# Performance work log

Hardware: AMD Instinct MI355X
Metric: run time of the kernel (lower is better)

Reference implementation:

```python
import jax, jax.numpy as jnp
import numpy as np
from jax import lax

B, C_IN, H = 64, 3, 64
K_FEAT, KSIZE, STRIDE = 24, 8, 8
G_IN, G_HID, F_HID, OUT = 52, 256, 256, 1


def setup_inputs() -> dict:
    key = jax.random.key(0)
    ks = jax.random.split(key, 8)
    s = lambda fan_in: 1.0 / np.sqrt(fan_in)
    return {
        "image": jax.random.normal(ks[0], (B, C_IN, H, H), jnp.float32),
        "conv_w": jax.random.normal(ks[1], (K_FEAT, C_IN, KSIZE, KSIZE), jnp.float32) * s(C_IN * KSIZE * KSIZE),
        "conv_b": jnp.zeros((K_FEAT,), jnp.float32),
        "g_w1": jax.random.normal(ks[2], (G_IN, G_HID), jnp.float32) * s(G_IN),
        "g_b1": jnp.zeros((G_HID,), jnp.float32),
        "g_w2": jax.random.normal(ks[3], (G_HID, G_HID), jnp.float32) * s(G_HID),
        "g_b2": jnp.zeros((G_HID,), jnp.float32),
        "f_w1": jax.random.normal(ks[4], (G_HID, F_HID), jnp.float32) * s(G_HID),
        "f_b1": jnp.zeros((F_HID,), jnp.float32),
        "f_w2": jax.random.normal(ks[5], (F_HID, OUT), jnp.float32) * s(F_HID),
        "f_b2": jnp.zeros((OUT,), jnp.float32),
    }


def reference(image, conv_w, conv_b, g_w1, g_b1, g_w2, g_b2, f_w1, f_b1, f_w2, f_b2):
    # feature_extractor: conv k8/s8 + ReLU -> (B, k, d, d)
    x = lax.conv_general_dilated(image, conv_w, (STRIDE, STRIDE), "VALID",
                                 dimension_numbers=("NCHW", "OIHW", "NCHW"))
    x = jax.nn.relu(x + conv_b[None, :, None, None])
    b, k, d, _ = x.shape
    # coordinate channels: x varies along columns, y along rows (linspace(-1,1,d))
    coord = jnp.linspace(-1.0, 1.0, d, dtype=x.dtype)
    cx = jnp.broadcast_to(coord[None, None, None, :], (b, 1, d, d))
    cy = jnp.broadcast_to(coord[None, None, :, None], (b, 1, d, d))
    x = jnp.concatenate([x, cx, cy], axis=1)          # (B, k+2, d, d)
    k2 = k + 2
    x = x.reshape(b, k2, d * d).transpose(0, 2, 1)     # (B, d^2, k+2)
    # all-pairs: pair (i, j) -> concat(x[:, j], x[:, i])  (matches repeat/cat in torch)
    left = jnp.broadcast_to(x[:, None, :, :], (b, d * d, d * d, k2))
    right = jnp.broadcast_to(x[:, :, None, :], (b, d * d, d * d, k2))
    pairs = jnp.concatenate([left, right], axis=-1)    # (B, d^2, d^2, 2(k+2))
    # g: shared MLP over pairs
    h = jax.nn.relu(pairs @ g_w1 + g_b1)
    h = jax.nn.relu(h @ g_w2 + g_b2)                   # (B, d^2, d^2, 256)
    pooled = jnp.sum(h, axis=(1, 2))                   # sum over d^4 pairs -> (B, 256)
    # f: head MLP
    h = jax.nn.relu(pooled @ f_w1 + f_b1)
    return h @ f_w2 + f_b2                             # (B, 1)
```

## Files before the change

### kernel.cpp

```cpp
#include <hip/hip_runtime.h>
#include <hip/hip_bf16.h>
#include <stdint.h>


typedef float f32x4 __attribute__((ext_vector_type(4)));
typedef float f32x2 __attribute__((ext_vector_type(2)));
typedef short short8 __attribute__((ext_vector_type(8)));
typedef int   int4v  __attribute__((ext_vector_type(4)));

__device__ __forceinline__ uint32_t cvt_pk_bf16(float lo, float hi) {
    uint32_t r;
    asm("v_cvt_pk_bf16_f32 %0, %1, %2" : "=v"(r) : "v"(lo), "v"(hi));
    return r;
}
__device__ __forceinline__ f32x2 relu2(f32x2 a) {
    f32x2 z = (f32x2){0.f, 0.f};
    return __builtin_elementwise_max(a, z);
}

__global__ void k12_front(const float* __restrict__ img, const float* __restrict__ cw,
                          const float* __restrict__ cb, const float* __restrict__ w1,
                          const float* __restrict__ b1, const float* __restrict__ w2,
                          float* __restrict__ u, float* __restrict__ v,
                          short* __restrict__ w2f) {
    int g = blockIdx.x;
    int t = threadIdx.x;
    if (g >= 256) {
        int fi = (g - 256) * 4 + (t >> 6);
        int l = t & 63;
        int ks = fi >> 4, ni2 = fi & 15;
        int n  = ni2 * 16 + (l & 15);
        int k0 = ks * 32 + (l >> 4) * 8;
        float f[8];
        #pragma unroll
        for (int e = 0; e < 8; ++e) f[e] = w2[(k0 + e) * 256 + n];
        union { short8 s; uint32_t w[4]; } A;
        A.w[0] = cvt_pk_bf16(f[0], f[1]);
        A.w[1] = cvt_pk_bf16(f[2], f[3]);
        A.w[2] = cvt_pk_bf16(f[4], f[5]);
        A.w[3] = cvt_pk_bf16(f[6], f[7]);
        *(short8*)(w2f + (fi * 64 + l) * 8) = A.s;
        return;
    }
    __shared__ float xs[16][26];
    int b = g >> 2, q = g & 3, p0 = q * 16;

    for (int idx = t; idx < 416; idx += 256) {
        int pl = idx / 26;
        int ch = idx - pl * 26;
        int pos = p0 + pl;
        int r = pos >> 3, c = pos & 7;
        float val;
        if (ch < 24) {
            float s = cb[ch];
            #pragma unroll
            for (int ci = 0; ci < 3; ++ci)
                #pragma unroll
                for (int kr = 0; kr < 8; ++kr) {
                    const float* ip = img + ((b * 3 + ci) * 64 + r * 8 + kr) * 64 + c * 8;
                    const float* wp = cw + ((ch * 3 + ci) * 8 + kr) * 8;
                    #pragma unroll
                    for (int kc = 0; kc < 8; ++kc) s += ip[kc] * wp[kc];
                }
            val = fmaxf(s, 0.f);
        } else if (ch == 24) {
            val = -1.f + (2.f / 7.f) * (float)c;
        } else {
            val = -1.f + (2.f / 7.f) * (float)r;
        }
        xs[pl][ch] = val;
    }
    __syncthreads();

    int c = t;
    float bc = b1[c];
    float su[16], sv[16];
    #pragma unroll
    for (int r = 0; r < 16; ++r) { su[r] = bc; sv[r] = 0.f; }
    #pragma unroll 2
    for (int k = 0; k < 26; ++k) {
        float wu = w1[k * 256 + c];
        float wv2 = w1[(26 + k) * 256 + c];
        #pragma unroll
        for (int r = 0; r < 16; ++r) {
            float xv = xs[r][k];
            su[r] += xv * wu;
            sv[r] += xv * wv2;
        }
    }
    #pragma unroll
    for (int r = 0; r < 16; ++r) {
        int bj = b * 64 + p0 + r;
        u[bj * 256 + c] = su[r];
        v[bj * 256 + c] = sv[r];
    }
}

#define STAGE_ALL(VSROW, WB)                                           \
{                                                                      \
    f32x4 va = *(const f32x4*)&vs[VSROW][col16 * 8];                   \
    f32x4 vb = *(const f32x4*)&vs[VSROW][col16 * 8 + 4];               \
    _Pragma("unroll 4")                                                \
    for (int p = 0; p < 8; ++p) {                                      \
        f32x4 x0 = *(const f32x4*)(uth + p * 2048);                    \
        f32x4 x1 = *(const f32x4*)(uth + p * 2048 + 4);                \
        f32x2 a0 = relu2((f32x2){x0.x, x0.y} + (f32x2){va.x, va.y});   \
        f32x2 a1 = relu2((f32x2){x0.z, x0.w} + (f32x2){va.z, va.w});   \
        f32x2 a2 = relu2((f32x2){x1.x, x1.y} + (f32x2){vb.x, vb.y});   \
        f32x2 a3 = relu2((f32x2){x1.z, x1.w} + (f32x2){vb.z, vb.w});   \
        int4v d;                                                       \
        d.x = (int)cvt_pk_bf16(a0.x, a0.y);                            \
        d.y = (int)cvt_pk_bf16(a1.x, a1.y);                            \
        d.z = (int)cvt_pk_bf16(a2.x, a2.y);                            \
        d.w = (int)cvt_pk_bf16(a3.x, a3.y);                            \
        *(int4v*)((WB) + p * 4096) = d;                                \
    }                                                                  \
}

#define MFMA_ROW(AV, MI, KS)                                                                    \
      acc[MI][0] = __builtin_amdgcn_mfma_f32_16x16x32_bf16(AV, Bf[KS][0], acc[MI][0], 0, 0, 0); \
      acc[MI][1] = __builtin_amdgcn_mfma_f32_16x16x32_bf16(AV, Bf[KS][1], acc[MI][1], 0, 0, 0); \
      acc[MI][2] = __builtin_amdgcn_mfma_f32_16x16x32_bf16(AV, Bf[KS][2], acc[MI][2], 0, 0, 0); \
      acc[MI][3] = __builtin_amdgcn_mfma_f32_16x16x32_bf16(AV, Bf[KS][3], acc[MI][3], 0, 0, 0);

#define MFMA_KS(KS)                                                   \
    { const char* hx = ((KS) & 1) ? hO : hE;                          \
      short8 a0 = *(const short8*)(hx + ((KS) >> 1) * 128);           \
      short8 a1 = *(const short8*)(hx + 8192  + ((KS) >> 1) * 128);   \
      short8 a2 = *(const short8*)(hx + 16384 + ((KS) >> 1) * 128);   \
      short8 a3 = *(const short8*)(hx + 24576 + ((KS) >> 1) * 128);   \
      MFMA_ROW(a0, 0, KS) MFMA_ROW(a1, 1, KS)                         \
      MFMA_ROW(a2, 2, KS) MFMA_ROW(a3, 3, KS) }

__global__ __launch_bounds__(256, 2) void k3_pairs(
        const float* __restrict__ u, const float* __restrict__ v,
        const short* __restrict__ w2f, const float* __restrict__ b2,
        float* __restrict__ part) {
    __shared__ short h1s[2][64 * 256];
    __shared__ float vs[8][256];
    int t = threadIdx.x;
    int lane = t & 63, wv = t >> 6;
    int lr = lane & 15, lg = lane >> 4;
    int blk = blockIdx.x;
    int b = blk & 63, i0 = (blk >> 6) * 8;
    bool late = (blk >> 8) & 1;

    {
        int q = t >> 5, c8 = (t & 31) * 8;
        const float* vr = v + (b * 64 + i0 + q) * 256 + c8;
        *(float4*)&vs[q][c8]     = *(const float4*)vr;
        *(float4*)&vs[q][c8 + 4] = *(const float4*)(vr + 4);
    }

    short8 Bf[8][4];
    #pragma unroll
    for (int ks = 0; ks < 8; ++ks)
        #pragma unroll
        for (int cg = 0; cg < 4; ++cg)
            Bf[ks][cg] = *(const short8*)(w2f + ((ks * 16 + wv * 4 + cg) * 64 + lane) * 8);

    f32x2 bias2[4];
    #pragma unroll
    for (int cg = 0; cg < 4; ++cg) {
        float bv = b2[wv * 64 + cg * 16 + lr];
        bias2[cg] = (f32x2){bv, bv};
    }

    int col16 = t & 31, rowbase = t >> 5;
    const float* uth = u + (b * 64 + rowbase) * 256 + col16 * 8;
    int wbase = rowbase * 512 + ((col16 * 16) ^ (rowbase << 4));
    int xb = (lg * 16) ^ ((lr & 7) << 4);
    int rE = lr * 512 + xb;
    int rO = lr * 512 + (xb ^ 64);

    __syncthreads();
    STAGE_ALL(0, (char*)h1s[0] + wbase)
    __syncthreads();

    f32x2 csum2[4];
    #pragma unroll
    for (int cg = 0; cg < 4; ++cg) csum2[cg] = (f32x2){0.f, 0.f};

    #pragma unroll 1
    for (int qq = 0; qq < 8; ++qq) {
        const char* hE = (const char*)h1s[qq & 1] + rE;
        const char* hO = (const char*)h1s[qq & 1] + rO;
        char* wb = (char*)h1s[(qq & 1) ^ 1] + wbase;

        f32x4 acc[4][4];
        #pragma unroll
        for (int mi = 0; mi < 4; ++mi)
            #pragma unroll
            for (int cg = 0; cg < 4; ++cg) acc[mi][cg] = (f32x4){0.f, 0.f, 0.f, 0.f};

        if (!late) {
            if (qq < 7) STAGE_ALL(qq + 1, wb)
            __builtin_amdgcn_s_setprio(1);
            MFMA_KS(0) MFMA_KS(1) MFMA_KS(2) MFMA_KS(3)
            MFMA_KS(4) MFMA_KS(5) MFMA_KS(6) MFMA_KS(7)
            __builtin_amdgcn_s_setprio(0);
        } else {
            __builtin_amdgcn_s_setprio(1);
            MFMA_KS(0) MFMA_KS(1) MFMA_KS(2) MFMA_KS(3)
            __builtin_amdgcn_s_setprio(0);
            if (qq < 7) STAGE_ALL(qq + 1, wb)
            __builtin_amdgcn_s_setprio(1);
            MFMA_KS(4) MFMA_KS(5) MFMA_KS(6) MFMA_KS(7)
            __builtin_amdgcn_s_setprio(0);
        }

        #pragma unroll
        for (int cg = 0; cg < 4; ++cg) {
            #pragma unroll
            for (int mi = 0; mi < 4; ++mi) {
                f32x2 lo = relu2((f32x2){acc[mi][cg].x, acc[mi][cg].y} + bias2[cg]);
                f32x2 hi = relu2((f32x2){acc[mi][cg].z, acc[mi][cg].w} + bias2[cg]);
                csum2[cg] = csum2[cg] + lo + hi;
            }
        }
        __syncthreads();
    }

    #pragma unroll
    for (int cg = 0; cg < 4; ++cg) {
        float s = csum2[cg].x + csum2[cg].y;
        s += __shfl_xor(s, 16);
        s += __shfl_xor(s, 32);
        if (lane < 16) part[blk * 256 + wv * 64 + cg * 16 + lr] = s;
    }
}

__global__ void k5_head(const float* __restrict__ part, const float* __restrict__ fw1,
                        const float* __restrict__ fb1, const float* __restrict__ fw2,
                        const float* __restrict__ fb2, float* __restrict__ out) {
    __shared__ float P[256];
    __shared__ float wsum[4];
    int b = blockIdx.x, t = threadIdx.x;
    float s0 = 0.f;
    #pragma unroll
    for (int g = 0; g < 8; ++g) s0 += part[(b + 64 * g) * 256 + t];
    P[t] = s0;
    __syncthreads();
    float a0 = 0.f, a1 = 0.f, a2 = 0.f, a3 = 0.f;
    for (int k = 0; k < 64; ++k) {
        a0 += P[k]       * fw1[k * 256 + t];
        a1 += P[k + 64]  * fw1[(k + 64) * 256 + t];
        a2 += P[k + 128] * fw1[(k + 128) * 256 + t];
        a3 += P[k + 192] * fw1[(k + 192) * 256 + t];
    }
    float h = fmaxf(fb1[t] + a0 + a1 + a2 + a3, 0.f);
    float p = h * fw2[t];
    #pragma unroll
    for (int off = 32; off >= 1; off >>= 1) p += __shfl_xor(p, off);
    if ((t & 63) == 0) wsum[t >> 6] = p;
    __syncthreads();
    if (t == 0) out[b] = wsum[0] + wsum[1] + wsum[2] + wsum[3] + fb2[0];
}

extern "C" void kernel_launch(void* const* d_in, const int* in_sizes, int n_in,
                              void* d_out, int out_size, void* d_ws, size_t ws_size,
                              hipStream_t stream) {
    const float* image  = (const float*)d_in[0];
    const float* conv_w = (const float*)d_in[1];
    const float* conv_b = (const float*)d_in[2];
    const float* g_w1   = (const float*)d_in[3];
    const float* g_b1   = (const float*)d_in[4];
    const float* g_w2   = (const float*)d_in[5];
    const float* g_b2   = (const float*)d_in[6];
    const float* f_w1   = (const float*)d_in[7];
    const float* f_b1   = (const float*)d_in[8];
    const float* f_w2   = (const float*)d_in[9];
    const float* f_b2   = (const float*)d_in[10];
    float* out = (float*)d_out;

    char* ws = (char*)d_ws;
    float* u    = (float*)(ws + 0);
    float* v    = (float*)(ws + 4194304);
    short* w2f  = (short*)(ws + 8388608);
    float* part = (float*)(ws + 8519680);

    k12_front<<<288, 256, 0, stream>>>(image, conv_w, conv_b, g_w1, g_b1, g_w2,
                                       u, v, w2f);
    k3_pairs<<<512, 256, 0, stream>>>(u, v, w2f, g_b2, part);
    k5_head<<<64, 256, 0, stream>>>(part, f_w1, f_b1, f_w2, f_b2, out);
}
```

Before: 66.39 us.

## Restructure pair kernel into 512-thread blocks with register-cached u rows

```diff
diff --git a/kernel.cpp b/kernel.cpp
--- a/kernel.cpp
+++ b/kernel.cpp
@@ -96,32 +96,24 @@
     }
 }
 
-#define STAGE_ALL(VSROW, WB)                                           \
+#define STAGE(Q, BUF)                                                  \
 {                                                                      \
-    f32x4 va = *(const f32x4*)&vs[VSROW][col16 * 8];                   \
-    f32x4 vb = *(const f32x4*)&vs[VSROW][col16 * 8 + 4];               \
-    _Pragma("unroll 4")                                                \
-    for (int p = 0; p < 8; ++p) {                                      \
-        f32x4 x0 = *(const f32x4*)(uth + p * 2048);                    \
-        f32x4 x1 = *(const f32x4*)(uth + p * 2048 + 4);                \
-        f32x2 a0 = relu2((f32x2){x0.x, x0.y} + (f32x2){va.x, va.y});   \
-        f32x2 a1 = relu2((f32x2){x0.z, x0.w} + (f32x2){va.z, va.w});   \
-        f32x2 a2 = relu2((f32x2){x1.x, x1.y} + (f32x2){vb.x, vb.y});   \
-        f32x2 a3 = relu2((f32x2){x1.z, x1.w} + (f32x2){vb.z, vb.w});   \
+    f32x4 va = *(const f32x4*)&vs[Q][col8 * 8];                        \
+    f32x4 vb = *(const f32x4*)&vs[Q][col8 * 8 + 4];                    \
+    _Pragma("unroll")                                                  \
+    for (int rr = 0; rr < 4; ++rr) {                                   \
+        f32x2 a0 = relu2((f32x2){u0[rr].x, u0[rr].y} + (f32x2){va.x, va.y}); \
+        f32x2 a1 = relu2((f32x2){u0[rr].z, u0[rr].w} + (f32x2){va.z, va.w}); \
+        f32x2 a2 = relu2((f32x2){u1[rr].x, u1[rr].y} + (f32x2){vb.x, vb.y}); \
+        f32x2 a3 = relu2((f32x2){u1[rr].z, u1[rr].w} + (f32x2){vb.z, vb.w}); \
         int4v d;                                                       \
         d.x = (int)cvt_pk_bf16(a0.x, a0.y);                            \
         d.y = (int)cvt_pk_bf16(a1.x, a1.y);                            \
         d.z = (int)cvt_pk_bf16(a2.x, a2.y);                            \
         d.w = (int)cvt_pk_bf16(a3.x, a3.y);                            \
-        *(int4v*)((WB) + p * 4096) = d;                                \
+        *(int4v*)((char*)(BUF) + wb[rr]) = d;                          \
     }                                                                  \
 }
-
-#define MFMA_ROW(AV, MI, KS)                                                                    \
-      acc[MI][0] = __builtin_amdgcn_mfma_f32_16x16x32_bf16(AV, Bf[KS][0], acc[MI][0], 0, 0, 0); \
-      acc[MI][1] = __builtin_amdgcn_mfma_f32_16x16x32_bf16(AV, Bf[KS][1], acc[MI][1], 0, 0, 0); \
-      acc[MI][2] = __builtin_amdgcn_mfma_f32_16x16x32_bf16(AV, Bf[KS][2], acc[MI][2], 0, 0, 0); \
-      acc[MI][3] = __builtin_amdgcn_mfma_f32_16x16x32_bf16(AV, Bf[KS][3], acc[MI][3], 0, 0, 0);
 
 #define MFMA_KS(KS)                                                   \
     { const char* hx = ((KS) & 1) ? hO : hE;                          \
@@ -129,21 +121,26 @@
       short8 a1 = *(const short8*)(hx + 8192  + ((KS) >> 1) * 128);   \
       short8 a2 = *(const short8*)(hx + 16384 + ((KS) >> 1) * 128);   \
       short8 a3 = *(const short8*)(hx + 24576 + ((KS) >> 1) * 128);   \
-      MFMA_ROW(a0, 0, KS) MFMA_ROW(a1, 1, KS)                         \
-      MFMA_ROW(a2, 2, KS) MFMA_ROW(a3, 3, KS) }
-
-__global__ __launch_bounds__(256, 2) void k3_pairs(
+      acc[0][0] = __builtin_amdgcn_mfma_f32_16x16x32_bf16(a0, Bf[KS][0], acc[0][0], 0, 0, 0); \
+      acc[1][0] = __builtin_amdgcn_mfma_f32_16x16x32_bf16(a1, Bf[KS][0], acc[1][0], 0, 0, 0); \
+      acc[2][0] = __builtin_amdgcn_mfma_f32_16x16x32_bf16(a2, Bf[KS][0], acc[2][0], 0, 0, 0); \
+      acc[3][0] = __builtin_amdgcn_mfma_f32_16x16x32_bf16(a3, Bf[KS][0], acc[3][0], 0, 0, 0); \
+      acc[0][1] = __builtin_amdgcn_mfma_f32_16x16x32_bf16(a0, Bf[KS][1], acc[0][1], 0, 0, 0); \
+      acc[1][1] = __builtin_amdgcn_mfma_f32_16x16x32_bf16(a1, Bf[KS][1], acc[1][1], 0, 0, 0); \
+      acc[2][1] = __builtin_amdgcn_mfma_f32_16x16x32_bf16(a2, Bf[KS][1], acc[2][1], 0, 0, 0); \
+      acc[3][1] = __builtin_amdgcn_mfma_f32_16x16x32_bf16(a3, Bf[KS][1], acc[3][1], 0, 0, 0); }
+
+__global__ __launch_bounds__(512, 2) void k3_pairs(
         const float* __restrict__ u, const float* __restrict__ v,
         const short* __restrict__ w2f, const float* __restrict__ b2,
         float* __restrict__ part) {
     __shared__ short h1s[2][64 * 256];
-    __shared__ float vs[8][256];
+    __shared__ float vs[16][256];
     int t = threadIdx.x;
     int lane = t & 63, wv = t >> 6;
     int lr = lane & 15, lg = lane >> 4;
     int blk = blockIdx.x;
-    int b = blk & 63, i0 = (blk >> 6) * 8;
-    bool late = (blk >> 8) & 1;
+    int b = blk & 63, i0 = (blk >> 6) * 16;
 
     {
         int q = t >> 5, c8 = (t & 31) * 8;
@@ -152,65 +149,64 @@
         *(float4*)&vs[q][c8 + 4] = *(const float4*)(vr + 4);
     }
 
-    short8 Bf[8][4];
+    short8 Bf[8][2];
     #pragma unroll
     for (int ks = 0; ks < 8; ++ks)
         #pragma unroll
-        for (int cg = 0; cg < 4; ++cg)
-            Bf[ks][cg] = *(const short8*)(w2f + ((ks * 16 + wv * 4 + cg) * 64 + lane) * 8);
-
-    f32x2 bias2[4];
-    #pragma unroll
-    for (int cg = 0; cg < 4; ++cg) {
-        float bv = b2[wv * 64 + cg * 16 + lr];
+        for (int cg = 0; cg < 2; ++cg)
+            Bf[ks][cg] = *(const short8*)(w2f + ((ks * 16 + wv * 2 + cg) * 64 + lane) * 8);
+
+    f32x2 bias2[2];
+    #pragma unroll
+    for (int cg = 0; cg < 2; ++cg) {
+        float bv = b2[wv * 32 + cg * 16 + lr];
         bias2[cg] = (f32x2){bv, bv};
     }
 
-    int col16 = t & 31, rowbase = t >> 5;
-    const float* uth = u + (b * 64 + rowbase) * 256 + col16 * 8;
-    int wbase = rowbase * 512 + ((col16 * 16) ^ (rowbase << 4));
-    int xb = (lg * 16) ^ ((lr & 7) << 4);
-    int rE = lr * 512 + xb;
-    int rO = lr * 512 + (xb ^ 64);
-
-    __syncthreads();
-    STAGE_ALL(0, (char*)h1s[0] + wbase)
-    __syncthreads();
-
-    f32x2 csum2[4];
-    #pragma unroll
-    for (int cg = 0; cg < 4; ++cg) csum2[cg] = (f32x2){0.f, 0.f};
+    int col8 = t & 31, rq = t >> 5;
+    const float* up = u + (b * 64 + rq * 4) * 256 + col8 * 8;
+    f32x4 u0[4], u1[4];
+    int wb[4];
+    #pragma unroll
+    for (int rr = 0; rr < 4; ++rr) {
+        u0[rr] = *(const f32x4*)(up + rr * 256);
+        u1[rr] = *(const f32x4*)(up + rr * 256 + 4);
+        int row = rq * 4 + rr;
+        wb[rr] = row * 512 + ((col8 * 16) ^ ((row & 7) << 4));
+    }
+
+    int XB = (lg * 16) ^ ((lr & 7) << 4);
+    int rE = lr * 512 + XB;
+    int rO = lr * 512 + (XB ^ 64);
+
+    __syncthreads();
+    STAGE(0, h1s[0])
+    __syncthreads();
+
+    f32x2 csum2[2];
+    csum2[0] = (f32x2){0.f, 0.f};
+    csum2[1] = (f32x2){0.f, 0.f};
 
     #pragma unroll 1
-    for (int qq = 0; qq < 8; ++qq) {
-        const char* hE = (const char*)h1s[qq & 1] + rE;
-        const char* hO = (const char*)h1s[qq & 1] + rO;
-        char* wb = (char*)h1s[(qq & 1) ^ 1] + wbase;
-
-        f32x4 acc[4][4];
+    for (int q = 0; q < 16; ++q) {
+        if (q < 15) STAGE(q + 1, h1s[(q + 1) & 1])
+
+        const char* hE = (const char*)h1s[q & 1] + rE;
+        const char* hO = (const char*)h1s[q & 1] + rO;
+
+        f32x4 acc[4][2];
         #pragma unroll
         for (int mi = 0; mi < 4; ++mi)
             #pragma unroll
-            for (int cg = 0; cg < 4; ++cg) acc[mi][cg] = (f32x4){0.f, 0.f, 0.f, 0.f};
-
-        if (!late) {
-            if (qq < 7) STAGE_ALL(qq + 1, wb)
-            __builtin_amdgcn_s_setprio(1);
-            MFMA_KS(0) MFMA_KS(1) MFMA_KS(2) MFMA_KS(3)
-            MFMA_KS(4) MFMA_KS(5) MFMA_KS(6) MFMA_KS(7)
-            __builtin_amdgcn_s_setprio(0);
-        } else {
-            __builtin_amdgcn_s_setprio(1);
-            MFMA_KS(0) MFMA_KS(1) MFMA_KS(2) MFMA_KS(3)
-            __builtin_amdgcn_s_setprio(0);
-            if (qq < 7) STAGE_ALL(qq + 1, wb)
-            __builtin_amdgcn_s_setprio(1);
-            MFMA_KS(4) MFMA_KS(5) MFMA_KS(6) MFMA_KS(7)
-            __builtin_amdgcn_s_setprio(0);
-        }
-
-        #pragma unroll
-        for (int cg = 0; cg < 4; ++cg) {
+            for (int cg = 0; cg < 2; ++cg) acc[mi][cg] = (f32x4){0.f, 0.f, 0.f, 0.f};
+
+        __builtin_amdgcn_s_setprio(1);
+        MFMA_KS(0) MFMA_KS(1) MFMA_KS(2) MFMA_KS(3)
+        MFMA_KS(4) MFMA_KS(5) MFMA_KS(6) MFMA_KS(7)
+        __builtin_amdgcn_s_setprio(0);
+
+        #pragma unroll
+        for (int cg = 0; cg < 2; ++cg) {
             #pragma unroll
             for (int mi = 0; mi < 4; ++mi) {
                 f32x2 lo = relu2((f32x2){acc[mi][cg].x, acc[mi][cg].y} + bias2[cg]);
@@ -222,11 +218,11 @@
     }
 
     #pragma unroll
-    for (int cg = 0; cg < 4; ++cg) {
+    for (int cg = 0; cg < 2; ++cg) {
         float s = csum2[cg].x + csum2[cg].y;
         s += __shfl_xor(s, 16);
         s += __shfl_xor(s, 32);
-        if (lane < 16) part[blk * 256 + wv * 64 + cg * 16 + lr] = s;
+        if (lane < 16) part[blk * 256 + wv * 32 + cg * 16 + lr] = s;
     }
 }
 
@@ -238,7 +234,7 @@
     int b = blockIdx.x, t = threadIdx.x;
     float s0 = 0.f;
     #pragma unroll
-    for (int g = 0; g < 8; ++g) s0 += part[(b + 64 * g) * 256 + t];
+    for (int g = 0; g < 4; ++g) s0 += part[(b + 64 * g) * 256 + t];
     P[t] = s0;
     __syncthreads();
     float a0 = 0.f, a1 = 0.f, a2 = 0.f, a3 = 0.f;
@@ -281,6 +277,6 @@
 
     k12_front<<<288, 256, 0, stream>>>(image, conv_w, conv_b, g_w1, g_b1, g_w2,
                                        u, v, w2f);
-    k3_pairs<<<512, 256, 0, stream>>>(u, v, w2f, g_b2, part);
+    k3_pairs<<<256, 512, 0, stream>>>(u, v, w2f, g_b2, part);
     k5_head<<<64, 256, 0, stream>>>(part, f_w1, f_b1, f_w2, f_b2, out);
 }
```

Measured after the change: 60.11 us. -9.5%, faster.
